# Kernel tuning notes

Measured on AMD Instinct MI355X. Metric: run time of the kernel, lower is better.

Reference implementation:

```python
import jax, jax.numpy as jnp
import numpy as np
from jax import lax

# Fixed-point scales (powers of two, as in linger's luna/venus pipeline).
# scale_gi = input_scale * weight_ih_scale, scale_gh = hidden_scale * weight_hh_scale.
SCALE_GI = 2.0 ** 14
SCALE_GH = 2.0 ** 14
Q27 = 2.0 ** 27
Q15 = 2.0 ** 15
Q31 = 2.0 ** 31
INT32_MIN = -(2.0 ** 31)
INT32_MAX = 2.0 ** 31 - 1


def quant_round(x, scale):
    # QuantMode.floor_add: floor(x*scale + 0.5)/scale, with straight-through gradient
    # (linger QAT rounding uses STE).
    q = jnp.floor(x * scale + 0.5) / scale
    return x + lax.stop_gradient(q - x)


@jax.custom_vjp
def qsigmoid(x):
    # Quantize input to Q27 int32, evaluate sigmoid, output Q31 -> requant to Q15.
    i_q27 = jnp.clip(jnp.floor(x * Q27 + 0.5), INT32_MIN, INT32_MAX)
    s = jax.nn.sigmoid(i_q27 / Q27)
    out_q31 = jnp.floor(s * Q31 + 0.5)
    out_q15 = jnp.floor(out_q31 * (2.0 ** -16) + 0.5)  # luna_requant(31 -> 15)
    return out_q15 / Q15

def _qsig_fwd(x):
    return qsigmoid(x), x

def _qsig_bwd(x, g):
    s = jax.nn.sigmoid(x)
    return (g * s * (1.0 - s),)

qsigmoid.defvjp(_qsig_fwd, _qsig_bwd)


@jax.custom_vjp
def qtanh(x):
    i_q27 = jnp.clip(jnp.floor(x * Q27 + 0.5), INT32_MIN, INT32_MAX)
    t = jnp.tanh(i_q27 / Q27)
    out_q31 = jnp.floor(t * Q31 + 0.5)
    out_q15 = jnp.floor(out_q31 * (2.0 ** -16) + 0.5)
    return out_q15 / Q15

def _qtanh_fwd(x):
    return qtanh(x), x

def _qtanh_bwd(x, g):
    t = jnp.tanh(x)
    return (g * (1.0 - t * t),)

qtanh.defvjp(_qtanh_fwd, _qtanh_bwd)


def setup_inputs() -> dict:
    key = jax.random.key(0)
    k = jax.random.split(key, 6)
    B, I, H = 8192, 512, 512
    return {
        "input_x": jax.random.normal(k[0], (B, I), dtype=jnp.float32),
        "hidden": jax.random.normal(k[1], (B, H), dtype=jnp.float32),
        "weight_ih": jax.random.normal(k[2], (3 * H, I), dtype=jnp.float32) * 0.05,
        "weight_hh": jax.random.normal(k[3], (3 * H, H), dtype=jnp.float32) * 0.05,
        "bias_ih": jax.random.normal(k[4], (3 * H,), dtype=jnp.float32) * 0.05,
        "bias_hh": jax.random.normal(k[5], (3 * H,), dtype=jnp.float32) * 0.05,
    }


def reference(input_x, hidden, weight_ih, weight_hh, bias_ih, bias_hh):
    # Dense gate projections: [B, 3H]
    gi = input_x @ weight_ih.T + bias_ih
    gh = hidden @ weight_hh.T + bias_hh
    # Requant gate pre-activations to fixed-point grid (biasih/biashh quantizers)
    gi = quant_round(gi, SCALE_GI)
    gh = quant_round(gh, SCALE_GH)
    i_r, i_i, i_n = jnp.split(gi, 3, axis=1)
    h_r, h_i, h_n = jnp.split(gh, 3, axis=1)
    resetgate = qsigmoid(i_r + h_r)
    inputgate = qsigmoid(i_i + h_i)
    # h_n requantized to Q27, reset*h_n product requantized to Q15
    h_n = quant_round(h_n, Q27)
    resetgate_h_n = quant_round(resetgate * h_n, Q15)
    newgate = qtanh(resetgate_h_n + i_n)
    new_hidden = quant_round(hidden, Q15)
    hy = newgate + inputgate * (new_hidden - newgate)
    return hy
```

## Files before the change

### kernel.cpp

```cpp
#include <hip/hip_runtime.h>
#include <math.h>


typedef _Float16 f16x8  __attribute__((ext_vector_type(8)));
typedef _Float16 f16x4  __attribute__((ext_vector_type(4)));
typedef __bf16   bf16x8 __attribute__((ext_vector_type(8)));
typedef float    f32x16 __attribute__((ext_vector_type(16)));

namespace {

constexpr int Bsz = 8192, Ksz = 512, Hsz = 512;
constexpr int BM = 64, BN = 64;

constexpr unsigned WCH0    = 16384u;
constexpr unsigned NCHUNK  = 16384u + 3072u;
constexpr unsigned WS_F16  = NCHUNK * 512u;
constexpr size_t   WS_NEED = (size_t)WS_F16 * 2;

__device__ __forceinline__ float qround(float x, float s, float invs) {
    return floorf(x * s + 0.5f) * invs;
}

__device__ __forceinline__ float qsigmoid_dev(float x) {
    float iq = floorf(x * 134217728.0f + 0.5f);
    iq = fminf(fmaxf(iq, -2147483648.0f), 2147483648.0f);
    float e = __expf(-iq * 7.450580596923828125e-9f);
    float s = __builtin_amdgcn_rcpf(1.0f + e);
    float q31 = floorf(s * 2147483648.0f + 0.5f);
    float q15 = floorf(q31 * 1.52587890625e-5f + 0.5f);
    return q15 * 3.0517578125e-5f;
}

__device__ __forceinline__ float qtanh_dev(float x) {
    float iq = floorf(x * 134217728.0f + 0.5f);
    iq = fminf(fmaxf(iq, -2147483648.0f), 2147483648.0f);
    float z = iq * 7.450580596923828125e-9f;
    float e = __expf(2.0f * z);
    float t = 1.0f - 2.0f * __builtin_amdgcn_rcpf(e + 1.0f);
    float q31 = floorf(t * 2147483648.0f + 0.5f);
    float q15 = floorf(q31 * 1.52587890625e-5f + 0.5f);
    return q15 * 3.0517578125e-5f;
}

__device__ __forceinline__ void dma16(const void* g, void* l) {
    __builtin_amdgcn_global_load_lds(
        (const __attribute__((address_space(1))) unsigned int*)g,
        (__attribute__((address_space(3))) unsigned int*)l, 16, 0, 0);
}

__device__ __forceinline__ void split2(float a, float b, unsigned& hi, unsigned& lo) {
    unsigned ua = __float_as_uint(a); ua += 0x7fffu + ((ua >> 16) & 1u);
    unsigned ub = __float_as_uint(b); ub += 0x7fffu + ((ub >> 16) & 1u);
    hi = (ua >> 16) | (ub & 0xffff0000u);
    float ra = a - __uint_as_float(ua & 0xffff0000u);
    float rb = b - __uint_as_float(ub & 0xffff0000u);
    unsigned va = __float_as_uint(ra); va += 0x7fffu + ((va >> 16) & 1u);
    unsigned vb = __float_as_uint(rb); vb += 0x7fffu + ((vb >> 16) & 1u);
    lo = (va >> 16) | (vb & 0xffff0000u);
}

}

__global__ __launch_bounds__(256) void cvt_lds_f16(
    const float* __restrict__ x, const float* __restrict__ h,
    const float* __restrict__ wih, const float* __restrict__ whh,
    _Float16* __restrict__ ws)
{
    __shared__ __align__(16) _Float16 lt[16384];

    const int b   = blockIdx.x;
    const int tid = threadIdx.x;

    const float* src;
    unsigned chbase;
    if (b < 512) {
        const int arr = b >> 8, M32 = b & 255;
        src = (arr ? h : x) + (size_t)M32 * 32u * 512u;
        chbase = (unsigned)arr * 8192u + (unsigned)M32 * 32u;
    } else {
        const int w = b - 512;
        const int g = w >> 4, N32 = w & 15;
        const int rowLocal = (g % 3) * 512 + N32 * 32;
        src = (g < 3 ? wih : whh) + (size_t)rowLocal * 512u;
        chbase = WCH0 + (unsigned)((g * 16 + N32) * 32);
    }

#pragma unroll
    for (int rep = 0; rep < 16; ++rep) {
        const int idx = rep * 256 + tid;
        const int row = idx >> 7;
        const int q   = idx & 127;
        const float4 v = *(const float4*)(src + (size_t)row * 512 + q * 4);
        const int K16  = q >> 2;
        const int kh   = (q >> 1) & 1;
        const int half = (q & 1) * 4;
        const int s    = q >> 1;
        const int rsw  = (row + s) & 31;
        f16x4 o;
        o[0] = (_Float16)v.x; o[1] = (_Float16)v.y;
        o[2] = (_Float16)v.z; o[3] = (_Float16)v.w;
        *(f16x4*)&lt[K16 * 512 + kh * 256 + rsw * 8 + half] = o;
    }
    __syncthreads();

    const int wid = tid >> 6, lane = tid & 63;
    const int kh  = lane >> 5, row = lane & 31;
#pragma unroll
    for (int cc = 0; cc < 8; ++cc) {
        const int K16 = wid * 8 + cc;
        const int rsw = (row + 2 * K16 + kh) & 31;
        const f16x8 o = *(const f16x8*)&lt[K16 * 512 + kh * 256 + rsw * 8];
        *(f16x8*)(ws + (size_t)(chbase + K16) * 512u + lane * 8) = o;
    }
}

__global__ __launch_bounds__(256, 2) void qgru_f16_dma2(
    const _Float16* __restrict__ ws, const float* __restrict__ hid,
    const float* __restrict__ bih, const float* __restrict__ bhh,
    float* __restrict__ out)
{
    __shared__ __align__(16) _Float16 lds[32768];

    const int t = threadIdx.x, lane = t & 63, wid = t >> 6;
    const int mt = wid >> 1, nt = wid & 1;
    const int m0 = blockIdx.x * BM, n0 = blockIdx.y * BN;

    unsigned goff[8];
    int      ldst[8];
    if (wid == 0) {
#pragma unroll
        for (int c = 0; c < 8; ++c) {
            int arr = c >> 2, mtc = (c >> 1) & 1, ks2 = c & 1;
            unsigned ch = (unsigned)arr * 8192u
                        + (unsigned)((m0 >> 5) + mtc) * 32u + (unsigned)ks2;
            goff[c] = ch * 1024u + (unsigned)lane * 16u;
            ldst[c] = (arr * 2 + mtc) * 1024 + ks2 * 512;
        }
    } else {
#pragma unroll
        for (int c = 0; c < 8; ++c) {
            int g = (wid - 1) * 2 + (c >> 2), ntc = (c >> 1) & 1, ks2 = c & 1;
            unsigned ch = WCH0
                        + (unsigned)((g * 16 + (n0 >> 5) + ntc) * 32) + (unsigned)ks2;
            goff[c] = ch * 1024u + (unsigned)lane * 16u;
            ldst[c] = 4096 + (g * 2 + ntc) * 1024 + ks2 * 512;
        }
    }

    f32x16 acc[6];
#pragma unroll
    for (int g = 0; g < 6; ++g)
#pragma unroll
        for (int i = 0; i < 16; ++i) acc[g][i] = 0.0f;

    const char* wsb = (const char*)ws;
    const int lr = lane & 31, lk8 = (lane >> 5) * 8;

#pragma unroll
    for (int c = 0; c < 8; ++c)
        dma16(wsb + goff[c], &lds[ldst[c]]);

    for (int step = 0; step < 16; ++step) {
        __syncthreads();

        if (step + 1 < 16) {
            const unsigned kb = (unsigned)(step + 1) * 2048u;
            const int nb = ((step + 1) & 1) * 16384;
#pragma unroll
            for (int c = 0; c < 8; ++c)
                dma16(wsb + goff[c] + kb, &lds[nb + ldst[c]]);
        }

        const int cb = (step & 1) * 16384;
#pragma unroll
        for (int ks2 = 0; ks2 < 2; ++ks2) {
            const int lfo = cb + ks2 * 512 + lk8 * 32 + lr * 8;
            const f16x8 ax = *(const f16x8*)&lds[lfo + (0 + mt) * 1024];
            const f16x8 ah = *(const f16x8*)&lds[lfo + (2 + mt) * 1024];
#pragma unroll
            for (int g = 0; g < 6; ++g) {
                const f16x8 b = *(const f16x8*)&lds[lfo + 4096 + (g * 2 + nt) * 1024];
                acc[g] = __builtin_amdgcn_mfma_f32_32x32x16_f16(
                             g < 3 ? ax : ah, b, acc[g], 0, 0, 0);
            }
        }
    }

    constexpr float S14 = 16384.0f,     I14 = 1.0f / 16384.0f;
    constexpr float S15 = 32768.0f,     I15 = 1.0f / 32768.0f;
    constexpr float S27 = 134217728.0f, I27 = 1.0f / 134217728.0f;

    const int lh = lane >> 5, l32 = lane & 31;
    const int n = n0 + nt * 32 + l32;
    const float br = bih[n], bi = bih[n + 512], bn = bih[n + 1024];
    const float cr = bhh[n], ci = bhh[n + 512], cn = bhh[n + 1024];

#pragma unroll
    for (int r = 0; r < 16; ++r) {
        const int row = (r & 3) + 8 * (r >> 2) + 4 * lh;
        const int m   = m0 + mt * 32 + row;
        const float hv = hid[(size_t)m * Hsz + n];

        float gir = qround(acc[0][r] + br, S14, I14);
        float gii = qround(acc[1][r] + bi, S14, I14);
        float gin = qround(acc[2][r] + bn, S14, I14);
        float ghr = qround(acc[3][r] + cr, S14, I14);
        float ghi = qround(acc[4][r] + ci, S14, I14);
        float ghn = qround(acc[5][r] + cn, S14, I14);
        float resetg = qsigmoid_dev(gir + ghr);
        float inputg = qsigmoid_dev(gii + ghi);
        float hn  = qround(ghn, S27, I27);
        float rh  = qround(resetg * hn, S15, I15);
        float newg = qtanh_dev(rh + gin);
        float nh  = qround(hv, S15, I15);
        out[(size_t)m * Hsz + n] = newg + inputg * (nh - newg);
    }
}

__global__ __launch_bounds__(256, 2) void qgru_mfma_bf16x3(
    const float* __restrict__ x, const float* __restrict__ hid,
    const float* __restrict__ wih, const float* __restrict__ whh,
    const float* __restrict__ bih, const float* __restrict__ bhh,
    float* __restrict__ out)
{
    __shared__ __align__(16) unsigned short lds[16384];

    const int t = threadIdx.x, lane = t & 63, wid = t >> 6;
    const int mt = wid >> 1, nt = wid & 1;
    const int m0 = blockIdx.x * BM, n0 = blockIdx.y * BN;
    const int s_r = t >> 2, s_k = (t & 3) << 2;
    const int s_kh = s_k >> 3, s_j = s_k & 7, s_rt = s_r >> 5, s_r32 = s_r & 31;

    const float* gA[2];
    gA[0] = x   + (size_t)(m0 + s_r) * Ksz + s_k;
    gA[1] = hid + (size_t)(m0 + s_r) * Ksz + s_k;
    const float* gW[6];
#pragma unroll
    for (int g = 0; g < 3; ++g) {
        gW[g]     = wih + (size_t)(g * Hsz + n0 + s_r) * Ksz + s_k;
        gW[g + 3] = whh + (size_t)(g * Hsz + n0 + s_r) * Ksz + s_k;
    }
    const int lh = lane >> 5, l32 = lane & 31;

    f32x16 acc[6];
#pragma unroll
    for (int g = 0; g < 6; ++g)
#pragma unroll
        for (int i = 0; i < 16; ++i) acc[g][i] = 0.0f;

    float4 vA[2], vW[6];
#pragma unroll
    for (int tt = 0; tt < 2; ++tt) vA[tt] = *(const float4*)gA[tt];
#pragma unroll
    for (int g = 0; g < 6; ++g)    vW[g]  = *(const float4*)gW[g];

    for (int k0 = 0; k0 < Ksz; k0 += 16) {
        __syncthreads();
#pragma unroll
        for (int tt = 0; tt < 2; ++tt) {
            unsigned h0, h1, l0, l1;
            split2(vA[tt].x, vA[tt].y, h0, l0);
            split2(vA[tt].z, vA[tt].w, h1, l1);
            unsigned bH = ((((tt*2+0)*2+s_rt)*2+s_kh)*32+s_r32)*8 + s_j;
            unsigned bL = ((((tt*2+1)*2+s_rt)*2+s_kh)*32+s_r32)*8 + s_j;
            *reinterpret_cast<uint2*>(&lds[bH]) = make_uint2(h0, h1);
            *reinterpret_cast<uint2*>(&lds[bL]) = make_uint2(l0, l1);
        }
#pragma unroll
        for (int g = 0; g < 6; ++g) {
            unsigned h0, h1, l0, l1;
            split2(vW[g].x, vW[g].y, h0, l0);
            split2(vW[g].z, vW[g].w, h1, l1);
            unsigned bH = 4096u + ((((g*2+0)*2+s_rt)*2+s_kh)*32+s_r32)*8 + s_j;
            unsigned bL = 4096u + ((((g*2+1)*2+s_rt)*2+s_kh)*32+s_r32)*8 + s_j;
            *reinterpret_cast<uint2*>(&lds[bH]) = make_uint2(h0, h1);
            *reinterpret_cast<uint2*>(&lds[bL]) = make_uint2(l0, l1);
        }
        __syncthreads();
        const int kn = (k0 + 16 < Ksz) ? (k0 + 16) : 0;
#pragma unroll
        for (int tt = 0; tt < 2; ++tt) vA[tt] = *(const float4*)(gA[tt] + kn);
#pragma unroll
        for (int g = 0; g < 6; ++g)    vW[g]  = *(const float4*)(gW[g] + kn);

        const bf16x8 ax_hi = *reinterpret_cast<const bf16x8*>(&lds[((((0)*2+mt)*2+lh)*32+l32)*8]);
        const bf16x8 ax_lo = *reinterpret_cast<const bf16x8*>(&lds[((((1)*2+mt)*2+lh)*32+l32)*8]);
        const bf16x8 ah_hi = *reinterpret_cast<const bf16x8*>(&lds[((((2)*2+mt)*2+lh)*32+l32)*8]);
        const bf16x8 ah_lo = *reinterpret_cast<const bf16x8*>(&lds[((((3)*2+mt)*2+lh)*32+l32)*8]);
#pragma unroll
        for (int g = 0; g < 6; ++g) {
            const bf16x8 b_hi = *reinterpret_cast<const bf16x8*>(&lds[4096u + ((((g*2+0)*2+nt)*2+lh)*32+l32)*8]);
            const bf16x8 b_lo = *reinterpret_cast<const bf16x8*>(&lds[4096u + ((((g*2+1)*2+nt)*2+lh)*32+l32)*8]);
            const bf16x8 a_hi = (g < 3) ? ax_hi : ah_hi;
            const bf16x8 a_lo = (g < 3) ? ax_lo : ah_lo;
            acc[g] = __builtin_amdgcn_mfma_f32_32x32x16_bf16(a_hi, b_hi, acc[g], 0, 0, 0);
            acc[g] = __builtin_amdgcn_mfma_f32_32x32x16_bf16(a_hi, b_lo, acc[g], 0, 0, 0);
            acc[g] = __builtin_amdgcn_mfma_f32_32x32x16_bf16(a_lo, b_hi, acc[g], 0, 0, 0);
        }
    }

    constexpr float S14 = 16384.0f,     I14 = 1.0f / 16384.0f;
    constexpr float S15 = 32768.0f,     I15 = 1.0f / 32768.0f;
    constexpr float S27 = 134217728.0f, I27 = 1.0f / 134217728.0f;
    const int n = n0 + nt * 32 + l32;
    const float br = bih[n], bi = bih[n + 512], bn = bih[n + 1024];
    const float cr = bhh[n], ci = bhh[n + 512], cn = bhh[n + 1024];
#pragma unroll
    for (int r = 0; r < 16; ++r) {
        const int row = (r & 3) + 8 * (r >> 2) + 4 * lh;
        const int m   = m0 + mt * 32 + row;
        const float hv = hid[(size_t)m * Hsz + n];
        float gir = qround(acc[0][r] + br, S14, I14);
        float gii = qround(acc[1][r] + bi, S14, I14);
        float gin = qround(acc[2][r] + bn, S14, I14);
        float ghr = qround(acc[3][r] + cr, S14, I14);
        float ghi = qround(acc[4][r] + ci, S14, I14);
        float ghn = qround(acc[5][r] + cn, S14, I14);
        float resetg = qsigmoid_dev(gir + ghr);
        float inputg = qsigmoid_dev(gii + ghi);
        float hn  = qround(ghn, S27, I27);
        float rh  = qround(resetg * hn, S15, I15);
        float newg = qtanh_dev(rh + gin);
        float nh  = qround(hv, S15, I15);
        out[(size_t)m * Hsz + n] = newg + inputg * (nh - newg);
    }
}

extern "C" void kernel_launch(void* const* d_in, const int* in_sizes, int n_in,
                              void* d_out, int out_size, void* d_ws, size_t ws_size,
                              hipStream_t stream) {
    const float* x   = (const float*)d_in[0];
    const float* hid = (const float*)d_in[1];
    const float* wih = (const float*)d_in[2];
    const float* whh = (const float*)d_in[3];
    const float* bih = (const float*)d_in[4];
    const float* bhh = (const float*)d_in[5];
    float* out = (float*)d_out;
    dim3 grid(Bsz / BM, Hsz / BN);

    if (ws_size >= WS_NEED) {
        cvt_lds_f16<<<512 + 96, 256, 0, stream>>>(
            x, hid, wih, whh, (_Float16*)d_ws);
        qgru_f16_dma2<<<grid, dim3(256), 0, stream>>>(
            (const _Float16*)d_ws, hid, bih, bhh, out);
    } else {
        qgru_mfma_bf16x3<<<grid, dim3(256), 0, stream>>>(
            x, hid, wih, whh, bih, bhh, out);
    }
}
```

Baseline: 131.4 us.

## Enlarge GEMM tile to 128x64, merge gate accumulators, XCD-aware block mapping

Each GEMM block now covers 128 rows instead of 64, so every B fragment read from LDS feeds two MFMAs. The x and h contributions for the reset and input gates now share one accumulator, which reduces accumulator count and epilogue work. Blocks are remapped so neighbouring tiles land on the same XCD. The main loop waits on explicit vmcnt, uses s_setprio and double barriers, and the conversion kernel splits K across twice as many blocks. The trade-offs are more LDS per block and rounding the gi+gh sum once instead of rounding each term separately, a small numeric deviation from the reference.

```diff
diff --git a/kernel.cpp b/kernel.cpp
--- a/kernel.cpp
+++ b/kernel.cpp
@@ -66,9 +66,11 @@
     const float* __restrict__ wih, const float* __restrict__ whh,
     _Float16* __restrict__ ws)
 {
-    __shared__ __align__(16) _Float16 lt[16384];
-
-    const int b   = blockIdx.x;
+    __shared__ __align__(16) _Float16 lt[8192];
+
+    const int b2  = blockIdx.x;
+    const int b   = b2 >> 1;
+    const int kha = b2 & 1;
     const int tid = threadIdx.x;
 
     const float* src;
@@ -84,136 +86,157 @@
         src = (g < 3 ? wih : whh) + (size_t)rowLocal * 512u;
         chbase = WCH0 + (unsigned)((g * 16 + N32) * 32);
     }
-
-#pragma unroll
-    for (int rep = 0; rep < 16; ++rep) {
+    src += kha * 256;
+
+#pragma unroll
+    for (int rep = 0; rep < 8; ++rep) {
         const int idx = rep * 256 + tid;
-        const int row = idx >> 7;
-        const int q   = idx & 127;
+        const int row = idx >> 6;
+        const int q   = idx & 63;
         const float4 v = *(const float4*)(src + (size_t)row * 512 + q * 4);
-        const int K16  = q >> 2;
+        const int K16l = q >> 2;
         const int kh   = (q >> 1) & 1;
         const int half = (q & 1) * 4;
-        const int s    = q >> 1;
-        const int rsw  = (row + s) & 31;
+        const int rsw  = (row + (q >> 1)) & 31;
         f16x4 o;
         o[0] = (_Float16)v.x; o[1] = (_Float16)v.y;
         o[2] = (_Float16)v.z; o[3] = (_Float16)v.w;
-        *(f16x4*)&lt[K16 * 512 + kh * 256 + rsw * 8 + half] = o;
+        *(f16x4*)&lt[K16l * 512 + kh * 256 + rsw * 8 + half] = o;
     }
     __syncthreads();
 
     const int wid = tid >> 6, lane = tid & 63;
     const int kh  = lane >> 5, row = lane & 31;
 #pragma unroll
-    for (int cc = 0; cc < 8; ++cc) {
-        const int K16 = wid * 8 + cc;
-        const int rsw = (row + 2 * K16 + kh) & 31;
-        const f16x8 o = *(const f16x8*)&lt[K16 * 512 + kh * 256 + rsw * 8];
-        *(f16x8*)(ws + (size_t)(chbase + K16) * 512u + lane * 8) = o;
-    }
-}
-
-__global__ __launch_bounds__(256, 2) void qgru_f16_dma2(
+    for (int cc = 0; cc < 4; ++cc) {
+        const int K16l = wid * 4 + cc;
+        const int rsw  = (row + 2 * K16l + kh) & 31;
+        const f16x8 o = *(const f16x8*)&lt[K16l * 512 + kh * 256 + rsw * 8];
+        *(f16x8*)(ws + (size_t)(chbase + (unsigned)(kha * 16 + K16l)) * 512u
+                      + lane * 8) = o;
+    }
+}
+
+__global__ __launch_bounds__(256, 2) void qgru_f16_dma3(
     const _Float16* __restrict__ ws, const float* __restrict__ hid,
     const float* __restrict__ bih, const float* __restrict__ bhh,
     float* __restrict__ out)
 {
-    __shared__ __align__(16) _Float16 lds[32768];
+    __shared__ __align__(16) _Float16 lds[40960];
 
     const int t = threadIdx.x, lane = t & 63, wid = t >> 6;
     const int mt = wid >> 1, nt = wid & 1;
-    const int m0 = blockIdx.x * BM, n0 = blockIdx.y * BN;
-
-    unsigned goff[8];
-    int      ldst[8];
-    if (wid == 0) {
-#pragma unroll
-        for (int c = 0; c < 8; ++c) {
-            int arr = c >> 2, mtc = (c >> 1) & 1, ks2 = c & 1;
-            unsigned ch = (unsigned)arr * 8192u
-                        + (unsigned)((m0 >> 5) + mtc) * 32u + (unsigned)ks2;
-            goff[c] = ch * 1024u + (unsigned)lane * 16u;
-            ldst[c] = (arr * 2 + mtc) * 1024 + ks2 * 512;
-        }
-    } else {
-#pragma unroll
-        for (int c = 0; c < 8; ++c) {
-            int g = (wid - 1) * 2 + (c >> 2), ntc = (c >> 1) & 1, ks2 = c & 1;
-            unsigned ch = WCH0
-                        + (unsigned)((g * 16 + (n0 >> 5) + ntc) * 32) + (unsigned)ks2;
-            goff[c] = ch * 1024u + (unsigned)lane * 16u;
-            ldst[c] = 4096 + (g * 2 + ntc) * 1024 + ks2 * 512;
-        }
-    }
-
-    f32x16 acc[6];
-#pragma unroll
-    for (int g = 0; g < 6; ++g)
-#pragma unroll
-        for (int i = 0; i < 16; ++i) acc[g][i] = 0.0f;
+
+    const int bid = blockIdx.x;
+    const int xcd = bid & 7, j = bid >> 3;
+    const int xw  = xcd + 8 * (j & 7);
+    const int yw  = j >> 3;
+    const int m0  = xw * 128, n0 = yw * 64;
+
+    unsigned goff[10];
+    int      ldst[10];
+#pragma unroll
+    for (int c = 0; c < 10; ++c) {
+        const int gi = wid * 10 + c;
+        unsigned ch; int lo;
+        if (gi < 16) {
+            const int arr = gi >> 3, m32 = (gi >> 1) & 3, ks2 = gi & 1;
+            ch = (unsigned)arr * 8192u
+               + (unsigned)((m0 >> 5) + m32) * 32u + (unsigned)ks2;
+            lo = ((arr * 4 + m32) * 2 + ks2) * 512;
+        } else {
+            const int bb = gi - 16;
+            const int g = bb >> 2, n32 = (bb >> 1) & 1, ks2 = bb & 1;
+            ch = WCH0 + (unsigned)((g * 16 + (n0 >> 5) + n32) * 32) + (unsigned)ks2;
+            lo = 8192 + ((g * 2 + n32) * 2 + ks2) * 512;
+        }
+        goff[c] = ch * 1024u + (unsigned)lane * 16u;
+        ldst[c] = lo;
+    }
+
+    f32x16 acc[4][2];
+#pragma unroll
+    for (int cid = 0; cid < 4; ++cid)
+#pragma unroll
+        for (int mf = 0; mf < 2; ++mf)
+#pragma unroll
+            for (int i = 0; i < 16; ++i) acc[cid][mf][i] = 0.0f;
 
     const char* wsb = (const char*)ws;
     const int lr = lane & 31, lk8 = (lane >> 5) * 8;
 
 #pragma unroll
-    for (int c = 0; c < 8; ++c)
+    for (int c = 0; c < 10; ++c)
         dma16(wsb + goff[c], &lds[ldst[c]]);
 
     for (int step = 0; step < 16; ++step) {
-        __syncthreads();
-
-        if (step + 1 < 16) {
+        const int cb = (step & 1) * 20480;
+
+        if (step < 15) {
             const unsigned kb = (unsigned)(step + 1) * 2048u;
-            const int nb = ((step + 1) & 1) * 16384;
-#pragma unroll
-            for (int c = 0; c < 8; ++c)
+            const int nb = ((step + 1) & 1) * 20480;
+#pragma unroll
+            for (int c = 0; c < 10; ++c)
                 dma16(wsb + goff[c] + kb, &lds[nb + ldst[c]]);
-        }
-
-        const int cb = (step & 1) * 16384;
+            asm volatile("s_waitcnt vmcnt(10)" ::: "memory");
+        } else {
+            asm volatile("s_waitcnt vmcnt(0)" ::: "memory");
+        }
+        __builtin_amdgcn_s_barrier();
+        asm volatile("" ::: "memory");
+        __builtin_amdgcn_s_setprio(1);
+
 #pragma unroll
         for (int ks2 = 0; ks2 < 2; ++ks2) {
             const int lfo = cb + ks2 * 512 + lk8 * 32 + lr * 8;
-            const f16x8 ax = *(const f16x8*)&lds[lfo + (0 + mt) * 1024];
-            const f16x8 ah = *(const f16x8*)&lds[lfo + (2 + mt) * 1024];
+            const f16x8 ax0 = *(const f16x8*)&lds[lfo + (mt * 2 + 0) * 1024];
+            const f16x8 ax1 = *(const f16x8*)&lds[lfo + (mt * 2 + 1) * 1024];
+            const f16x8 ah0 = *(const f16x8*)&lds[lfo + (4 + mt * 2 + 0) * 1024];
+            const f16x8 ah1 = *(const f16x8*)&lds[lfo + (4 + mt * 2 + 1) * 1024];
 #pragma unroll
             for (int g = 0; g < 6; ++g) {
-                const f16x8 b = *(const f16x8*)&lds[lfo + 4096 + (g * 2 + nt) * 1024];
-                acc[g] = __builtin_amdgcn_mfma_f32_32x32x16_f16(
-                             g < 3 ? ax : ah, b, acc[g], 0, 0, 0);
+                const f16x8 bv = *(const f16x8*)&lds[lfo + 8192 + (g * 2 + nt) * 1024];
+                const int cid = (g < 3) ? g : (g == 5 ? 3 : g - 3);
+                const f16x8 a0 = (g < 3) ? ax0 : ah0;
+                const f16x8 a1 = (g < 3) ? ax1 : ah1;
+                acc[cid][0] = __builtin_amdgcn_mfma_f32_32x32x16_f16(
+                                  a0, bv, acc[cid][0], 0, 0, 0);
+                acc[cid][1] = __builtin_amdgcn_mfma_f32_32x32x16_f16(
+                                  a1, bv, acc[cid][1], 0, 0, 0);
             }
         }
+
+        __builtin_amdgcn_s_setprio(0);
+        asm volatile("" ::: "memory");
+        __builtin_amdgcn_s_barrier();
     }
 
     constexpr float S14 = 16384.0f,     I14 = 1.0f / 16384.0f;
     constexpr float S15 = 32768.0f,     I15 = 1.0f / 32768.0f;
-    constexpr float S27 = 134217728.0f, I27 = 1.0f / 134217728.0f;
 
     const int lh = lane >> 5, l32 = lane & 31;
     const int n = n0 + nt * 32 + l32;
-    const float br = bih[n], bi = bih[n + 512], bn = bih[n + 1024];
-    const float cr = bhh[n], ci = bhh[n + 512], cn = bhh[n + 1024];
-
-#pragma unroll
-    for (int r = 0; r < 16; ++r) {
-        const int row = (r & 3) + 8 * (r >> 2) + 4 * lh;
-        const int m   = m0 + mt * 32 + row;
-        const float hv = hid[(size_t)m * Hsz + n];
-
-        float gir = qround(acc[0][r] + br, S14, I14);
-        float gii = qround(acc[1][r] + bi, S14, I14);
-        float gin = qround(acc[2][r] + bn, S14, I14);
-        float ghr = qround(acc[3][r] + cr, S14, I14);
-        float ghi = qround(acc[4][r] + ci, S14, I14);
-        float ghn = qround(acc[5][r] + cn, S14, I14);
-        float resetg = qsigmoid_dev(gir + ghr);
-        float inputg = qsigmoid_dev(gii + ghi);
-        float hn  = qround(ghn, S27, I27);
-        float rh  = qround(resetg * hn, S15, I15);
-        float newg = qtanh_dev(rh + gin);
-        float nh  = qround(hv, S15, I15);
-        out[(size_t)m * Hsz + n] = newg + inputg * (nh - newg);
+    const float brc = bih[n] + bhh[n];
+    const float bic = bih[n + 512] + bhh[n + 512];
+    const float bnn = bih[n + 1024];
+    const float cnn = bhh[n + 1024];
+
+#pragma unroll
+    for (int mf = 0; mf < 2; ++mf) {
+#pragma unroll
+        for (int r = 0; r < 16; ++r) {
+            const int row = (r & 3) + 8 * (r >> 2) + 4 * lh;
+            const int m   = m0 + mt * 64 + mf * 32 + row;
+            const float hv = hid[(size_t)m * Hsz + n];
+            const float rg  = qsigmoid_dev(qround(acc[0][mf][r] + brc, S14, I14));
+            const float ig  = qsigmoid_dev(qround(acc[1][mf][r] + bic, S14, I14));
+            const float gin = qround(acc[2][mf][r] + bnn, S14, I14);
+            const float ghn = qround(acc[3][mf][r] + cnn, S14, I14);
+            const float rh  = qround(rg * ghn, S15, I15);
+            const float ng  = qtanh_dev(rh + gin);
+            const float nh  = qround(hv, S15, I15);
+            out[(size_t)m * Hsz + n] = ng + ig * (nh - ng);
+        }
     }
 }
 
@@ -336,14 +359,14 @@
     const float* bih = (const float*)d_in[4];
     const float* bhh = (const float*)d_in[5];
     float* out = (float*)d_out;
-    dim3 grid(Bsz / BM, Hsz / BN);
 
     if (ws_size >= WS_NEED) {
-        cvt_lds_f16<<<512 + 96, 256, 0, stream>>>(
+        cvt_lds_f16<<<1216, 256, 0, stream>>>(
             x, hid, wih, whh, (_Float16*)d_ws);
-        qgru_f16_dma2<<<grid, dim3(256), 0, stream>>>(
+        qgru_f16_dma3<<<512, 256, 0, stream>>>(
             (const _Float16*)d_ws, hid, bih, bhh, out);
     } else {
+        dim3 grid(Bsz / BM, Hsz / BN);
         qgru_mfma_bf16x3<<<grid, dim3(256), 0, stream>>>(
             x, hid, wih, whh, bih, bhh, out);
     }
```

Result: faster. 126.2 us (-3.9%).

## Halve K-step LDS footprint to raise GEMM occupancy and split conversion blocks

Applied to the files above, without the earlier changes.

The main GEMM kernel now stages a single 16-wide K chunk per step instead of two. This halves its LDS buffer (32 KB instead of 64 KB double-buffered), lets launch bounds target 4 blocks per CU, and doubles the number of pipeline steps. The DMA issue is now spread evenly across all four waves. The f16 conversion kernel is split into two blocks per tile, one per K half, each using half the LDS. This raises conversion parallelism. The trade-off is more barriers per GEMM and possible register pressure from the tighter launch bound with six 16-float accumulators.

```diff
diff --git a/kernel.cpp b/kernel.cpp
--- a/kernel.cpp
+++ b/kernel.cpp
@@ -66,9 +66,11 @@
     const float* __restrict__ wih, const float* __restrict__ whh,
     _Float16* __restrict__ ws)
 {
-    __shared__ __align__(16) _Float16 lt[16384];
-
-    const int b   = blockIdx.x;
+    __shared__ __align__(16) _Float16 lt[8192];
+
+    const int b2  = blockIdx.x;
+    const int b   = b2 >> 1;
+    const int kha = b2 & 1;
     const int tid = threadIdx.x;
 
     const float* src;
@@ -84,67 +86,65 @@
         src = (g < 3 ? wih : whh) + (size_t)rowLocal * 512u;
         chbase = WCH0 + (unsigned)((g * 16 + N32) * 32);
     }
-
-#pragma unroll
-    for (int rep = 0; rep < 16; ++rep) {
+    src += kha * 256;
+
+#pragma unroll
+    for (int rep = 0; rep < 8; ++rep) {
         const int idx = rep * 256 + tid;
-        const int row = idx >> 7;
-        const int q   = idx & 127;
+        const int row = idx >> 6;
+        const int q   = idx & 63;
         const float4 v = *(const float4*)(src + (size_t)row * 512 + q * 4);
-        const int K16  = q >> 2;
+        const int K16l = q >> 2;
         const int kh   = (q >> 1) & 1;
         const int half = (q & 1) * 4;
-        const int s    = q >> 1;
-        const int rsw  = (row + s) & 31;
+        const int rsw  = (row + (q >> 1)) & 31;
         f16x4 o;
         o[0] = (_Float16)v.x; o[1] = (_Float16)v.y;
         o[2] = (_Float16)v.z; o[3] = (_Float16)v.w;
-        *(f16x4*)&lt[K16 * 512 + kh * 256 + rsw * 8 + half] = o;
+        *(f16x4*)&lt[K16l * 512 + kh * 256 + rsw * 8 + half] = o;
     }
     __syncthreads();
 
     const int wid = tid >> 6, lane = tid & 63;
     const int kh  = lane >> 5, row = lane & 31;
 #pragma unroll
-    for (int cc = 0; cc < 8; ++cc) {
-        const int K16 = wid * 8 + cc;
-        const int rsw = (row + 2 * K16 + kh) & 31;
-        const f16x8 o = *(const f16x8*)&lt[K16 * 512 + kh * 256 + rsw * 8];
-        *(f16x8*)(ws + (size_t)(chbase + K16) * 512u + lane * 8) = o;
-    }
-}
-
-__global__ __launch_bounds__(256, 2) void qgru_f16_dma2(
+    for (int cc = 0; cc < 4; ++cc) {
+        const int K16l = wid * 4 + cc;
+        const int rsw  = (row + 2 * K16l + kh) & 31;
+        const f16x8 o = *(const f16x8*)&lt[K16l * 512 + kh * 256 + rsw * 8];
+        *(f16x8*)(ws + (size_t)(chbase + (unsigned)(kha * 16 + K16l)) * 512u
+                      + lane * 8) = o;
+    }
+}
+
+__global__ __launch_bounds__(256, 4) void qgru_f16_occ(
     const _Float16* __restrict__ ws, const float* __restrict__ hid,
     const float* __restrict__ bih, const float* __restrict__ bhh,
     float* __restrict__ out)
 {
-    __shared__ __align__(16) _Float16 lds[32768];
+    __shared__ __align__(16) _Float16 lds[16384];
 
     const int t = threadIdx.x, lane = t & 63, wid = t >> 6;
     const int mt = wid >> 1, nt = wid & 1;
     const int m0 = blockIdx.x * BM, n0 = blockIdx.y * BN;
 
-    unsigned goff[8];
-    int      ldst[8];
-    if (wid == 0) {
-#pragma unroll
-        for (int c = 0; c < 8; ++c) {
-            int arr = c >> 2, mtc = (c >> 1) & 1, ks2 = c & 1;
-            unsigned ch = (unsigned)arr * 8192u
-                        + (unsigned)((m0 >> 5) + mtc) * 32u + (unsigned)ks2;
-            goff[c] = ch * 1024u + (unsigned)lane * 16u;
-            ldst[c] = (arr * 2 + mtc) * 1024 + ks2 * 512;
-        }
-    } else {
-#pragma unroll
-        for (int c = 0; c < 8; ++c) {
-            int g = (wid - 1) * 2 + (c >> 2), ntc = (c >> 1) & 1, ks2 = c & 1;
-            unsigned ch = WCH0
-                        + (unsigned)((g * 16 + (n0 >> 5) + ntc) * 32) + (unsigned)ks2;
-            goff[c] = ch * 1024u + (unsigned)lane * 16u;
-            ldst[c] = 4096 + (g * 2 + ntc) * 1024 + ks2 * 512;
-        }
+    unsigned goff[4];
+    int      ldst[4];
+#pragma unroll
+    for (int c = 0; c < 4; ++c) {
+        const int idx = wid * 4 + c;
+        unsigned ch; int lo;
+        if (idx < 4) {
+            const int arr = idx >> 1, mtc = idx & 1;
+            ch = (unsigned)arr * 8192u + (unsigned)((m0 >> 5) + mtc) * 32u;
+            lo = idx * 512;
+        } else {
+            const int w = idx - 4, g = w >> 1, ntc = w & 1;
+            ch = WCH0 + (unsigned)((g * 16 + (n0 >> 5) + ntc) * 32);
+            lo = 2048 + w * 512;
+        }
+        goff[c] = ch * 1024u + (unsigned)lane * 16u;
+        ldst[c] = lo;
     }
 
     f32x16 acc[6];
@@ -157,32 +157,29 @@
     const int lr = lane & 31, lk8 = (lane >> 5) * 8;
 
 #pragma unroll
-    for (int c = 0; c < 8; ++c)
+    for (int c = 0; c < 4; ++c)
         dma16(wsb + goff[c], &lds[ldst[c]]);
 
-    for (int step = 0; step < 16; ++step) {
+    for (int step = 0; step < 32; ++step) {
         __syncthreads();
 
-        if (step + 1 < 16) {
-            const unsigned kb = (unsigned)(step + 1) * 2048u;
-            const int nb = ((step + 1) & 1) * 16384;
-#pragma unroll
-            for (int c = 0; c < 8; ++c)
+        if (step + 1 < 32) {
+            const unsigned kb = (unsigned)(step + 1) * 1024u;
+            const int nb = ((step + 1) & 1) * 8192;
+#pragma unroll
+            for (int c = 0; c < 4; ++c)
                 dma16(wsb + goff[c] + kb, &lds[nb + ldst[c]]);
         }
 
-        const int cb = (step & 1) * 16384;
-#pragma unroll
-        for (int ks2 = 0; ks2 < 2; ++ks2) {
-            const int lfo = cb + ks2 * 512 + lk8 * 32 + lr * 8;
-            const f16x8 ax = *(const f16x8*)&lds[lfo + (0 + mt) * 1024];
-            const f16x8 ah = *(const f16x8*)&lds[lfo + (2 + mt) * 1024];
-#pragma unroll
-            for (int g = 0; g < 6; ++g) {
-                const f16x8 b = *(const f16x8*)&lds[lfo + 4096 + (g * 2 + nt) * 1024];
-                acc[g] = __builtin_amdgcn_mfma_f32_32x32x16_f16(
-                             g < 3 ? ax : ah, b, acc[g], 0, 0, 0);
-            }
+        const int cb = (step & 1) * 8192;
+        const int lfo = cb + lk8 * 32 + lr * 8;
+        const f16x8 ax = *(const f16x8*)&lds[lfo + (0 + mt) * 512];
+        const f16x8 ah = *(const f16x8*)&lds[lfo + (2 + mt) * 512];
+#pragma unroll
+        for (int g = 0; g < 6; ++g) {
+            const f16x8 b = *(const f16x8*)&lds[lfo + 2048 + (g * 2 + nt) * 512];
+            acc[g] = __builtin_amdgcn_mfma_f32_32x32x16_f16(
+                         g < 3 ? ax : ah, b, acc[g], 0, 0, 0);
         }
     }
 
@@ -339,9 +336,9 @@
     dim3 grid(Bsz / BM, Hsz / BN);
 
     if (ws_size >= WS_NEED) {
-        cvt_lds_f16<<<512 + 96, 256, 0, stream>>>(
+        cvt_lds_f16<<<1216, 256, 0, stream>>>(
             x, hid, wih, whh, (_Float16*)d_ws);
-        qgru_f16_dma2<<<grid, dim3(256), 0, stream>>>(
+        qgru_f16_occ<<<grid, dim3(256), 0, stream>>>(
             (const _Float16*)d_ws, hid, bih, bhh, out);
     } else {
         qgru_mfma_bf16x3<<<grid, dim3(256), 0, stream>>>(
```

Result: no change. 129.9 us (-1.2%).
